# Kernel tuning notes

Measured on AMD Instinct MI355X. Metric: run time of the kernel, lower is better.

Reference implementation:

```python
import jax, jax.numpy as jnp
import numpy as np

NH, NP, NL, ED = 8, 8, 1, 256  # num_heads, num_sam_pts, num_levels, embed_dim
EPS = 1e-5


def setup_inputs() -> dict:
    key = jax.random.key(0)
    ks = jax.random.split(key, 6)
    bs, h, w = 8, 64, 64
    d = ED // NH
    return {
        "query": jax.random.normal(ks[0], (bs, 1, ED), jnp.float32),
        "single_feat": jax.random.normal(ks[1], (bs, h * w, NH, d), jnp.float32),
        "ref_2d": jax.random.uniform(ks[2], (bs, h * w, NL, 2), jnp.float32),
        "W_off": jax.random.normal(ks[3], (ED, NH * NL * NP * 2), jnp.float32) * 0.02,
        "b_off": jnp.zeros((NH * NL * NP * 2,), jnp.float32),
        "W_attn": jax.random.normal(ks[4], (ED, NH * NL * NP), jnp.float32) * 0.02,
        "b_attn": jnp.zeros((NH * NL * NP,), jnp.float32),
        "ln_g": jnp.ones((ED,), jnp.float32),
        "ln_b": jnp.zeros((ED,), jnp.float32),
        "h": h,
        "w": w,
    }


def reference(query, single_feat, ref_2d, W_off, b_off, W_attn, b_attn, ln_g, ln_b, h, w):
    bs, nq, _, d = single_feat.shape
    # query: [bs,1,ED] repeated over all h*w query positions
    q = jnp.broadcast_to(query, (bs, h * w, ED))

    # sampling offsets (relu'd, normalized by (w,h)) added to reference points
    off = jax.nn.relu(q @ W_off + b_off).reshape(bs, nq, NH, NL, NP, 2)
    offset_normalizer = jnp.array([w, h], dtype=q.dtype)  # (w, h) order as in torch
    loc = ref_2d[:, :, None, :, None, :] + off / offset_normalizer  # [bs,nq,NH,NL,NP,2]

    # attention weights: relu then softmax over points (last axis)
    aw = jax.nn.relu(q @ W_attn + b_attn).reshape(bs, nq, NH, NL, NP)
    aw = jax.nn.softmax(aw, axis=-1)

    # single-level bilinear grid_sample (align_corners=False, zero padding)
    g = 2.0 * loc[:, :, :, 0] - 1.0  # level 0 -> [bs,nq,NH,NP,2]
    x = (g[..., 0] + 1.0) * (w / 2.0) - 0.5  # pixel coords
    y = (g[..., 1] + 1.0) * (h / 2.0) - 0.5
    x0 = jnp.floor(x)
    y0 = jnp.floor(y)
    x0i = x0.astype(jnp.int32)
    y0i = y0.astype(jnp.int32)

    v = single_feat.transpose(0, 2, 1, 3)  # [bs,NH,H*W,d]

    def gather(xi, yi):
        valid = (xi >= 0) & (xi < w) & (yi >= 0) & (yi < h)  # [bs,nq,NH,NP]
        idx = jnp.clip(yi, 0, h - 1) * w + jnp.clip(xi, 0, w - 1)
        idx = idx.transpose(0, 2, 1, 3).reshape(bs, NH, nq * NP, 1)
        s = jnp.take_along_axis(v, idx, axis=2).reshape(bs, NH, nq, NP, d)
        return s * valid.transpose(0, 2, 1, 3)[..., None].astype(s.dtype)

    wx = (x - x0).transpose(0, 2, 1, 3)[..., None]  # [bs,NH,nq,NP,1]
    wy = (y - y0).transpose(0, 2, 1, 3)[..., None]
    s00 = gather(x0i, y0i)
    s01 = gather(x0i + 1, y0i)
    s10 = gather(x0i, y0i + 1)
    s11 = gather(x0i + 1, y0i + 1)
    top = s00 * (1.0 - wx) + s01 * wx
    bot = s10 * (1.0 - wx) + s11 * wx
    sampled = top * (1.0 - wy) + bot * wy  # [bs,NH,nq,NP,d]

    # weighted sum over points, merge heads
    out = jnp.einsum('bhqpd,bqhp->bqhd', sampled, aw[:, :, :, 0]).reshape(bs, nq, NH * d)

    # norm(dropout(output) + query) -- dropout is identity in eval mode
    res = out + q
    mu = res.mean(-1, keepdims=True)
    var = res.var(-1, keepdims=True)
    return (res - mu) / jnp.sqrt(var + EPS) * ln_g + ln_b
```

## Files before the change

### kernel.cpp

```cpp
#include <hip/hip_runtime.h>

#define ED 256
#define NHEAD 8
#define NPTS 8
#define DHEAD 32
#define QPB 8

__global__ __launch_bounds__(256) void precompute_kernel(
    const float* __restrict__ query,
    const float* __restrict__ W_off, const float* __restrict__ b_off,
    const float* __restrict__ W_attn, const float* __restrict__ b_attn,
    float* __restrict__ ws)
{
    const int b = blockIdx.x;
    const int t = threadIdx.x;
    __shared__ float sq[ED];
    __shared__ float sattn[NHEAD * NPTS];

    sq[t] = query[b * ED + t];
    __syncthreads();

    if (t < 128) {
        float a0 = 0.f, a1 = 0.f, a2 = 0.f, a3 = 0.f;
        #pragma unroll 4
        for (int k = 0; k < ED; k += 4) {
            a0 = fmaf(sq[k + 0], W_off[(k + 0) * 128 + t], a0);
            a1 = fmaf(sq[k + 1], W_off[(k + 1) * 128 + t], a1);
            a2 = fmaf(sq[k + 2], W_off[(k + 2) * 128 + t], a2);
            a3 = fmaf(sq[k + 3], W_off[(k + 3) * 128 + t], a3);
        }
        ws[b * 192 + t] = fmaxf(b_off[t] + ((a0 + a1) + (a2 + a3)), 0.0f);
    } else if (t < 192) {
        const int j = t - 128;
        float a0 = 0.f, a1 = 0.f, a2 = 0.f, a3 = 0.f;
        #pragma unroll 4
        for (int k = 0; k < ED; k += 4) {
            a0 = fmaf(sq[k + 0], W_attn[(k + 0) * 64 + j], a0);
            a1 = fmaf(sq[k + 1], W_attn[(k + 1) * 64 + j], a1);
            a2 = fmaf(sq[k + 2], W_attn[(k + 2) * 64 + j], a2);
            a3 = fmaf(sq[k + 3], W_attn[(k + 3) * 64 + j], a3);
        }
        sattn[j] = fmaxf(b_attn[j] + ((a0 + a1) + (a2 + a3)), 0.0f);
    }
    __syncthreads();

    if (t >= 128 && t < 192) {
        const int j = t - 128;
        const int hh = j >> 3;
        float m = -1e30f;
        #pragma unroll
        for (int p = 0; p < NPTS; ++p) m = fmaxf(m, sattn[hh * NPTS + p]);
        float s = 0.0f;
        #pragma unroll
        for (int p = 0; p < NPTS; ++p) s += expf(sattn[hh * NPTS + p] - m);
        ws[b * 192 + 128 + j] = expf(sattn[j] - m) / s;
    }
}

__global__ __launch_bounds__(256) void deform_attn_kernel(
    const float* __restrict__ feat,
    const float* __restrict__ ref2d,
    const float* __restrict__ query,
    const float* __restrict__ ln_g, const float* __restrict__ ln_b,
    const float* __restrict__ ws,
    const int* __restrict__ Hp, const int* __restrict__ Wp,
    float* __restrict__ out,
    int nq, int bs)
{
    const int blk = blockIdx.x;
    const int b = blk % bs;
    const int qbase = (blk / bs) * QPB;
    const int t = threadIdx.x;

    __shared__ float s_off[128];
    __shared__ float s_aw[64];
    __shared__ float s_ref[QPB * 2];
    __shared__ __align__(16) float s_c[QPB * 64 * 8];

    if (t < 128)      s_off[t] = ws[b * 192 + t];
    else if (t < 192) s_aw[t - 128] = ws[b * 192 + t];
    else if (t < 192 + QPB * 2) {
        const int i = t - 192;
        s_ref[i] = ref2d[(b * nq + qbase + (i >> 1)) * 2 + (i & 1)];
    }
    const int H = Hp[0];
    const int W = Wp[0];
    __syncthreads();

    #pragma unroll
    for (int u = t; u < QPB * 64; u += 256) {
        const int qL = u >> 6;
        const int hp = u & 63;
        const int p  = hp & 7;
        const int h  = hp >> 3;

        const float x = s_ref[qL * 2 + 0] * (float)W - 0.5f + s_off[hp * 2 + 0];
        const float y = s_ref[qL * 2 + 1] * (float)H - 0.5f + s_off[hp * 2 + 1];
        const float aw = s_aw[hp];

        const float xf = floorf(x);
        const float yf = floorf(y);
        const int ix = (int)xf;
        const int iy = (int)yf;
        const float wx = x - xf;
        const float wy = y - yf;

        const bool vx0 = (ix >= 0) && (ix < W);
        const bool vx1 = (ix + 1 >= 0) && (ix + 1 < W);
        const bool vy0 = (iy >= 0) && (iy < H);
        const bool vy1 = (iy + 1 >= 0) && (iy + 1 < H);
        const int cx0 = min(max(ix, 0), W - 1);
        const int cx1 = min(max(ix + 1, 0), W - 1);
        const int cy0 = min(max(iy, 0), H - 1);
        const int cy1 = min(max(iy + 1, 0), H - 1);

        const int r0 = cy0 * W;
        const int r1 = cy1 * W;
        int4 idx;
        idx.x = r0 + cx0;
        idx.y = r0 + cx1;
        idx.z = r1 + cx0;
        idx.w = r1 + cx1;

        const float awx = aw * wx, awix = aw - awx;
        float4 wt;
        wt.x = (vx0 && vy0) ? awix * (1.0f - wy) : 0.0f;
        wt.y = (vx1 && vy0) ? awx  * (1.0f - wy) : 0.0f;
        wt.z = (vx0 && vy1) ? awix * wy          : 0.0f;
        wt.w = (vx1 && vy1) ? awx  * wy          : 0.0f;

        const int e = (qL * 64 + p * 8 + h) * 8;
        *(int4*)  (&s_c[e])     = idx;
        *(float4*)(&s_c[e + 4]) = wt;
    }
    __syncthreads();

    const int qL   = t >> 6;
    const int lane = t & 63;
    const int h    = lane >> 3;
    const int c4   = lane & 7;

    const float* fb = feat + (size_t)b * nq * ED + h * DHEAD + c4 * 4;
    const float4 qv = *(const float4*)(query + b * ED + lane * 4);
    const float4 g  = *(const float4*)(ln_g + lane * 4);
    const float4 be = *(const float4*)(ln_b + lane * 4);

    #pragma unroll
    for (int gq = 0; gq < QPB / 4; ++gq) {
        const int qloc = gq * 4 + qL;
        const int q = qbase + qloc;
        const int cb = qloc * 512;

        float ax = 0.f, ay = 0.f, az = 0.f, aw4 = 0.f;

        int4   idxA = *(const int4*)  (&s_c[cb + h * 8]);
        float4 wtA  = *(const float4*)(&s_c[cb + h * 8 + 4]);
        float4 v0 = *(const float4*)(fb + (size_t)idxA.x * ED);
        float4 v1 = *(const float4*)(fb + (size_t)idxA.y * ED);
        float4 v2 = *(const float4*)(fb + (size_t)idxA.z * ED);
        float4 v3 = *(const float4*)(fb + (size_t)idxA.w * ED);

        #pragma unroll
        for (int p = 0; p < NPTS; ++p) {
            int4 idxB; float4 wtB;
            float4 u0, u1, u2, u3;
            if (p < NPTS - 1) {
                const int e = cb + (p + 1) * 64 + h * 8;
                idxB = *(const int4*)  (&s_c[e]);
                wtB  = *(const float4*)(&s_c[e + 4]);
                u0 = *(const float4*)(fb + (size_t)idxB.x * ED);
                u1 = *(const float4*)(fb + (size_t)idxB.y * ED);
                u2 = *(const float4*)(fb + (size_t)idxB.z * ED);
                u3 = *(const float4*)(fb + (size_t)idxB.w * ED);
            }
            ax = fmaf(wtA.x, v0.x, ax); ay = fmaf(wtA.x, v0.y, ay);
            az = fmaf(wtA.x, v0.z, az); aw4 = fmaf(wtA.x, v0.w, aw4);
            ax = fmaf(wtA.y, v1.x, ax); ay = fmaf(wtA.y, v1.y, ay);
            az = fmaf(wtA.y, v1.z, az); aw4 = fmaf(wtA.y, v1.w, aw4);
            ax = fmaf(wtA.z, v2.x, ax); ay = fmaf(wtA.z, v2.y, ay);
            az = fmaf(wtA.z, v2.z, az); aw4 = fmaf(wtA.z, v2.w, aw4);
            ax = fmaf(wtA.w, v3.x, ax); ay = fmaf(wtA.w, v3.y, ay);
            az = fmaf(wtA.w, v3.z, az); aw4 = fmaf(wtA.w, v3.w, aw4);
            if (p < NPTS - 1) {
                idxA = idxB; wtA = wtB;
                v0 = u0; v1 = u1; v2 = u2; v3 = u3;
            }
        }

        const float r0 = ax + qv.x;
        const float r1 = ay + qv.y;
        const float r2 = az + qv.z;
        const float r3 = aw4 + qv.w;

        float s  = (r0 + r1) + (r2 + r3);
        float ss = fmaf(r0, r0, fmaf(r1, r1, fmaf(r2, r2, r3 * r3)));
        #pragma unroll
        for (int m = 1; m < 64; m <<= 1) {
            s  += __shfl_xor(s, m, 64);
            ss += __shfl_xor(ss, m, 64);
        }
        const float mean = s * (1.0f / ED);
        const float var  = ss * (1.0f / ED) - mean * mean;
        const float inv  = rsqrtf(var + 1e-5f);

        float4 o;
        o.x = (r0 - mean) * inv * g.x + be.x;
        o.y = (r1 - mean) * inv * g.y + be.y;
        o.z = (r2 - mean) * inv * g.z + be.z;
        o.w = (r3 - mean) * inv * g.w + be.w;
        *(float4*)(out + ((size_t)b * nq + q) * ED + lane * 4) = o;
    }
}

extern "C" void kernel_launch(void* const* d_in, const int* in_sizes, int n_in,
                              void* d_out, int out_size, void* d_ws, size_t ws_size,
                              hipStream_t stream)
{
    const float* query  = (const float*)d_in[0];
    const float* feat   = (const float*)d_in[1];
    const float* ref2d  = (const float*)d_in[2];
    const float* W_off  = (const float*)d_in[3];
    const float* b_off  = (const float*)d_in[4];
    const float* W_attn = (const float*)d_in[5];
    const float* b_attn = (const float*)d_in[6];
    const float* ln_g   = (const float*)d_in[7];
    const float* ln_b   = (const float*)d_in[8];
    const int*   Hp     = (const int*)d_in[9];
    const int*   Wp     = (const int*)d_in[10];
    float* out = (float*)d_out;
    float* ws  = (float*)d_ws;

    const int bs = in_sizes[0] / ED;
    const int nq = in_sizes[2] / (bs * 2);

    precompute_kernel<<<bs, 256, 0, stream>>>(query, W_off, b_off, W_attn, b_attn, ws);
    deform_attn_kernel<<<bs * nq / QPB, 256, 0, stream>>>(feat, ref2d, query, ln_g, ln_b,
                                                          ws, Hp, Wp, out, nq, bs);
}
```

Measured before the change: 146.6 us.

## Split precompute matvec across all threads, use SoA sample table, batch gathers in pairs

The precompute kernel now spreads the offset and attention matvecs over all 256 threads with K-split partial sums reduced through shared memory, instead of leaving 64 threads idle. The deform kernel stores sample indices and weights as separate int4/float4 arrays with a point-major layout. It replaces the software-pipelined per-point loop with pairs of points, issuing eight gathers at once, and adds a min-4-blocks launch bound. This aims to raise memory-level parallelism in the gather phase, at the cost of possible register pressure under the occupancy bound.

```diff
diff --git a/kernel.cpp b/kernel.cpp
--- a/kernel.cpp
+++ b/kernel.cpp
@@ -15,49 +15,65 @@
     const int b = blockIdx.x;
     const int t = threadIdx.x;
     __shared__ float sq[ED];
-    __shared__ float sattn[NHEAD * NPTS];
+    __shared__ float red[256];
+    __shared__ float sattn[64];
 
     sq[t] = query[b * ED + t];
     __syncthreads();
 
-    if (t < 128) {
+    {
+        const int col  = t & 127;
+        const int half = t >> 7;
+        const float* Wp = W_off + (size_t)half * 128 * 128 + col;
+        const float* qp = sq + half * 128;
         float a0 = 0.f, a1 = 0.f, a2 = 0.f, a3 = 0.f;
-        #pragma unroll 4
-        for (int k = 0; k < ED; k += 4) {
-            a0 = fmaf(sq[k + 0], W_off[(k + 0) * 128 + t], a0);
-            a1 = fmaf(sq[k + 1], W_off[(k + 1) * 128 + t], a1);
-            a2 = fmaf(sq[k + 2], W_off[(k + 2) * 128 + t], a2);
-            a3 = fmaf(sq[k + 3], W_off[(k + 3) * 128 + t], a3);
-        }
-        ws[b * 192 + t] = fmaxf(b_off[t] + ((a0 + a1) + (a2 + a3)), 0.0f);
-    } else if (t < 192) {
-        const int j = t - 128;
+        #pragma unroll 8
+        for (int k = 0; k < 128; k += 4) {
+            a0 = fmaf(qp[k + 0], Wp[(k + 0) * 128], a0);
+            a1 = fmaf(qp[k + 1], Wp[(k + 1) * 128], a1);
+            a2 = fmaf(qp[k + 2], Wp[(k + 2) * 128], a2);
+            a3 = fmaf(qp[k + 3], Wp[(k + 3) * 128], a3);
+        }
+        red[t] = (a0 + a1) + (a2 + a3);
+    }
+    __syncthreads();
+    if (t < 128) ws[b * 192 + t] = fmaxf(red[t] + red[t + 128] + b_off[t], 0.0f);
+    __syncthreads();
+
+    {
+        const int col = t & 63;
+        const int qtr = t >> 6;
+        const float* Wp = W_attn + (size_t)qtr * 64 * 64 + col;
+        const float* qp = sq + qtr * 64;
         float a0 = 0.f, a1 = 0.f, a2 = 0.f, a3 = 0.f;
-        #pragma unroll 4
-        for (int k = 0; k < ED; k += 4) {
-            a0 = fmaf(sq[k + 0], W_attn[(k + 0) * 64 + j], a0);
-            a1 = fmaf(sq[k + 1], W_attn[(k + 1) * 64 + j], a1);
-            a2 = fmaf(sq[k + 2], W_attn[(k + 2) * 64 + j], a2);
-            a3 = fmaf(sq[k + 3], W_attn[(k + 3) * 64 + j], a3);
-        }
-        sattn[j] = fmaxf(b_attn[j] + ((a0 + a1) + (a2 + a3)), 0.0f);
-    }
-    __syncthreads();
-
-    if (t >= 128 && t < 192) {
-        const int j = t - 128;
-        const int hh = j >> 3;
+        #pragma unroll 8
+        for (int k = 0; k < 64; k += 4) {
+            a0 = fmaf(qp[k + 0], Wp[(k + 0) * 64], a0);
+            a1 = fmaf(qp[k + 1], Wp[(k + 1) * 64], a1);
+            a2 = fmaf(qp[k + 2], Wp[(k + 2) * 64], a2);
+            a3 = fmaf(qp[k + 3], Wp[(k + 3) * 64], a3);
+        }
+        red[t] = (a0 + a1) + (a2 + a3);
+    }
+    __syncthreads();
+    if (t < 64) {
+        sattn[t] = fmaxf(red[t] + red[t + 64] + red[t + 128] + red[t + 192]
+                         + b_attn[t], 0.0f);
+    }
+    __syncthreads();
+    if (t < 64) {
+        const int hh = t >> 3;
         float m = -1e30f;
         #pragma unroll
         for (int p = 0; p < NPTS; ++p) m = fmaxf(m, sattn[hh * NPTS + p]);
         float s = 0.0f;
         #pragma unroll
         for (int p = 0; p < NPTS; ++p) s += expf(sattn[hh * NPTS + p] - m);
-        ws[b * 192 + 128 + j] = expf(sattn[j] - m) / s;
+        ws[b * 192 + 128 + t] = expf(sattn[t] - m) / s;
     }
 }
 
-__global__ __launch_bounds__(256) void deform_attn_kernel(
+__global__ __launch_bounds__(256, 4) void deform_attn_kernel(
     const float* __restrict__ feat,
     const float* __restrict__ ref2d,
     const float* __restrict__ query,
@@ -75,7 +91,8 @@
     __shared__ float s_off[128];
     __shared__ float s_aw[64];
     __shared__ float s_ref[QPB * 2];
-    __shared__ __align__(16) float s_c[QPB * 64 * 8];
+    __shared__ int4   s_idx[QPB * 64];
+    __shared__ float4 s_wt [QPB * 64];
 
     if (t < 128)      s_off[t] = ws[b * 192 + t];
     else if (t < 192) s_aw[t - 128] = ws[b * 192 + t];
@@ -90,9 +107,10 @@
     #pragma unroll
     for (int u = t; u < QPB * 64; u += 256) {
         const int qL = u >> 6;
-        const int hp = u & 63;
-        const int p  = hp & 7;
-        const int h  = hp >> 3;
+        const int l  = u & 63;
+        const int p  = l >> 3;
+        const int h  = l & 7;
+        const int hp = h * 8 + p;
 
         const float x = s_ref[qL * 2 + 0] * (float)W - 0.5f + s_off[hp * 2 + 0];
         const float y = s_ref[qL * 2 + 1] * (float)H - 0.5f + s_off[hp * 2 + 1];
@@ -129,9 +147,8 @@
         wt.z = (vx0 && vy1) ? awix * wy          : 0.0f;
         wt.w = (vx1 && vy1) ? awx  * wy          : 0.0f;
 
-        const int e = (qL * 64 + p * 8 + h) * 8;
-        *(int4*)  (&s_c[e])     = idx;
-        *(float4*)(&s_c[e + 4]) = wt;
+        s_idx[u] = idx;
+        s_wt[u]  = wt;
     }
     __syncthreads();
 
@@ -149,42 +166,43 @@
     for (int gq = 0; gq < QPB / 4; ++gq) {
         const int qloc = gq * 4 + qL;
         const int q = qbase + qloc;
-        const int cb = qloc * 512;
+        const int cb = qloc * 64 + h;
 
         float ax = 0.f, ay = 0.f, az = 0.f, aw4 = 0.f;
 
-        int4   idxA = *(const int4*)  (&s_c[cb + h * 8]);
-        float4 wtA  = *(const float4*)(&s_c[cb + h * 8 + 4]);
-        float4 v0 = *(const float4*)(fb + (size_t)idxA.x * ED);
-        float4 v1 = *(const float4*)(fb + (size_t)idxA.y * ED);
-        float4 v2 = *(const float4*)(fb + (size_t)idxA.z * ED);
-        float4 v3 = *(const float4*)(fb + (size_t)idxA.w * ED);
-
-        #pragma unroll
-        for (int p = 0; p < NPTS; ++p) {
-            int4 idxB; float4 wtB;
-            float4 u0, u1, u2, u3;
-            if (p < NPTS - 1) {
-                const int e = cb + (p + 1) * 64 + h * 8;
-                idxB = *(const int4*)  (&s_c[e]);
-                wtB  = *(const float4*)(&s_c[e + 4]);
-                u0 = *(const float4*)(fb + (size_t)idxB.x * ED);
-                u1 = *(const float4*)(fb + (size_t)idxB.y * ED);
-                u2 = *(const float4*)(fb + (size_t)idxB.z * ED);
-                u3 = *(const float4*)(fb + (size_t)idxB.w * ED);
-            }
-            ax = fmaf(wtA.x, v0.x, ax); ay = fmaf(wtA.x, v0.y, ay);
-            az = fmaf(wtA.x, v0.z, az); aw4 = fmaf(wtA.x, v0.w, aw4);
-            ax = fmaf(wtA.y, v1.x, ax); ay = fmaf(wtA.y, v1.y, ay);
-            az = fmaf(wtA.y, v1.z, az); aw4 = fmaf(wtA.y, v1.w, aw4);
-            ax = fmaf(wtA.z, v2.x, ax); ay = fmaf(wtA.z, v2.y, ay);
-            az = fmaf(wtA.z, v2.z, az); aw4 = fmaf(wtA.z, v2.w, aw4);
-            ax = fmaf(wtA.w, v3.x, ax); ay = fmaf(wtA.w, v3.y, ay);
-            az = fmaf(wtA.w, v3.z, az); aw4 = fmaf(wtA.w, v3.w, aw4);
-            if (p < NPTS - 1) {
-                idxA = idxB; wtA = wtB;
-                v0 = u0; v1 = u1; v2 = u2; v3 = u3;
-            }
+        #pragma unroll
+        for (int pp = 0; pp < NPTS; pp += 2) {
+            const int4   iA = s_idx[cb + pp * 8];
+            const float4 wA = s_wt [cb + pp * 8];
+            const int4   iB = s_idx[cb + pp * 8 + 8];
+            const float4 wB = s_wt [cb + pp * 8 + 8];
+
+            const float4 a0 = *(const float4*)(fb + (size_t)iA.x * ED);
+            const float4 a1 = *(const float4*)(fb + (size_t)iA.y * ED);
+            const float4 a2 = *(const float4*)(fb + (size_t)iA.z * ED);
+            const float4 a3 = *(const float4*)(fb + (size_t)iA.w * ED);
+            const float4 b0 = *(const float4*)(fb + (size_t)iB.x * ED);
+            const float4 b1 = *(const float4*)(fb + (size_t)iB.y * ED);
+            const float4 b2 = *(const float4*)(fb + (size_t)iB.z * ED);
+            const float4 b3 = *(const float4*)(fb + (size_t)iB.w * ED);
+
+            ax = fmaf(wA.x, a0.x, ax); ay = fmaf(wA.x, a0.y, ay);
+            az = fmaf(wA.x, a0.z, az); aw4 = fmaf(wA.x, a0.w, aw4);
+            ax = fmaf(wA.y, a1.x, ax); ay = fmaf(wA.y, a1.y, ay);
+            az = fmaf(wA.y, a1.z, az); aw4 = fmaf(wA.y, a1.w, aw4);
+            ax = fmaf(wA.z, a2.x, ax); ay = fmaf(wA.z, a2.y, ay);
+            az = fmaf(wA.z, a2.z, az); aw4 = fmaf(wA.z, a2.w, aw4);
+            ax = fmaf(wA.w, a3.x, ax); ay = fmaf(wA.w, a3.y, ay);
+            az = fmaf(wA.w, a3.z, az); aw4 = fmaf(wA.w, a3.w, aw4);
+
+            ax = fmaf(wB.x, b0.x, ax); ay = fmaf(wB.x, b0.y, ay);
+            az = fmaf(wB.x, b0.z, az); aw4 = fmaf(wB.x, b0.w, aw4);
+            ax = fmaf(wB.y, b1.x, ax); ay = fmaf(wB.y, b1.y, ay);
+            az = fmaf(wB.y, b1.z, az); aw4 = fmaf(wB.y, b1.w, aw4);
+            ax = fmaf(wB.z, b2.x, ax); ay = fmaf(wB.z, b2.y, ay);
+            az = fmaf(wB.z, b2.z, az); aw4 = fmaf(wB.z, b2.w, aw4);
+            ax = fmaf(wB.w, b3.x, ax); ay = fmaf(wB.w, b3.y, ay);
+            az = fmaf(wB.w, b3.z, az); aw4 = fmaf(wB.w, b3.w, aw4);
         }
 
         const float r0 = ax + qv.x;
```

Result: no change. 145.0 us (-1.1%).
